# Optimization experiments

Measured on AMD Instinct MI355X. Metric: run time of the kernel, lower is better.

The kernel has to match this reference:

```python
import jax, jax.numpy as jnp
import numpy as np

B, S, D_IN = 4, 2048, 1024
D_OUT, H = 1024, 16
HD = D_OUT // H  # head_dim = 64

def setup_inputs() -> dict:
    key = jax.random.key(0)
    ks = jax.random.split(key, 6)
    scale_in = 1.0 / np.sqrt(D_IN)
    scale_out = 1.0 / np.sqrt(D_OUT)
    return {
        "x": jax.random.normal(ks[0], (B, S, D_IN), dtype=jnp.float32),
        "Wq": jax.random.uniform(ks[1], (D_OUT, D_IN), jnp.float32, -scale_in, scale_in),
        "Wk": jax.random.uniform(ks[2], (D_OUT, D_IN), jnp.float32, -scale_in, scale_in),
        "Wv": jax.random.uniform(ks[3], (D_OUT, D_IN), jnp.float32, -scale_in, scale_in),
        "Wo": jax.random.uniform(ks[4], (D_OUT, D_OUT), jnp.float32, -scale_out, scale_out),
        "bo": jax.random.uniform(ks[5], (D_OUT,), jnp.float32, -scale_out, scale_out),
    }

def reference(x, Wq, Wk, Wv, Wo, bo):
    b, s, _ = x.shape
    # projections (nn.Linear: x @ W.T), split into heads -> [b, h, s, hd]
    def proj(W):
        return jnp.einsum('bsd,ed->bse', x, W).reshape(b, s, H, HD).transpose(0, 2, 1, 3)
    q, k, v = proj(Wq), proj(Wk), proj(Wv)
    # full score matrix [b, h, s, s] with causal mask, scaled softmax
    scores = jnp.einsum('bhqd,bhkd->bhqk', q, k)
    causal = jnp.tril(jnp.ones((s, s), dtype=bool))
    scores = jnp.where(causal, scores, -jnp.inf)
    attn = jax.nn.softmax(scores / np.sqrt(HD), axis=-1)
    # dropout p=0.0 -> identity
    ctx = jnp.einsum('bhqk,bhkd->bqhd', attn, v).reshape(b, s, D_OUT)
    return jnp.einsum('bsd,ed->bse', ctx, Wo) + bo
```

## Files before the change

### kernel.cpp

```cpp
#include <hip/hip_runtime.h>
#include <cstdint>
#include <cstddef>

#define S_LEN   2048
#define D_MODEL 1024
#define N_HEADS 16
#define HEAD_DIM 64
#define BATCH   4
#define M_ROWS  (BATCH * S_LEN)

typedef _Float16 half8  __attribute__((ext_vector_type(8)));
typedef _Float16 half4v __attribute__((ext_vector_type(4)));
typedef float    float4v __attribute__((ext_vector_type(4)));

#define AS1 __attribute__((address_space(1)))
#define AS3 __attribute__((address_space(3)))

#define QSCL 0.1803368801111832f

__device__ __forceinline__ int swz(int row, int byteInRow) {
    return row * 128 + ((((byteInRow >> 4) ^ (row & 7)) << 4)) + (byteInRow & 15);
}

__device__ __forceinline__ int vperm(int a) {
    return (a & 0x20) | ((a & 0x0C) << 1) | ((a & 0x10) >> 2) | (a & 3);
}

__global__ __launch_bounds__(256) void cvt_all(const float* __restrict__ x,
                                               const float* __restrict__ wq,
                                               const float* __restrict__ wk,
                                               const float* __restrict__ wv,
                                               const float* __restrict__ wo,
                                               _Float16* __restrict__ dst) {
    const int NX = M_ROWS * D_MODEL / 4;
    const int NW = D_MODEL * D_MODEL / 4;
    int i = blockIdx.x * 256 + threadIdx.x;
    int j = i;
    const float4v* src;
    if (j < NX) src = (const float4v*)x;
    else {
        j -= NX;
        if (j < NW) src = (const float4v*)wq;
        else { j -= NW;
            if (j < NW) src = (const float4v*)wk;
            else { j -= NW;
                if (j < NW) src = (const float4v*)wv;
                else { j -= NW; src = (const float4v*)wo; }
            }
        }
    }
    float4v v = src[j];
    half4v h;
    h[0] = (_Float16)v[0]; h[1] = (_Float16)v[1];
    h[2] = (_Float16)v[2]; h[3] = (_Float16)v[3];
    ((half4v*)dst)[i] = h;
}

#define GK   1024
#define GNT  16
#define BUFB 49152
#define GEMM_LDS (3 * BUFB)

template <int MODE>
__global__ __launch_bounds__(512, 2) void gemm8p(const _Float16* __restrict__ A,
                                                 const _Float16* __restrict__ Bw,
                                                 _Float16* __restrict__ O1,
                                                 _Float16* __restrict__ O2,
                                                 float* __restrict__ Of,
                                                 const float* __restrict__ bias,
                                                 int N) {
    extern __shared__ char smem[];

    const int tid  = threadIdx.x;
    const int wave = tid >> 6;
    const int lane = tid & 63;
    const int quad = lane >> 4;
    const int l16  = lane & 15;
    const int wm   = wave >> 1;
    const int wn   = wave & 1;

    const int rowBase = blockIdx.x * 256;
    const int colBase = blockIdx.y * 128;

    const int srow = tid >> 3;
    const int csw  = ((tid & 7) ^ (srow & 7)) * 8;
    const _Float16* aS[4];
    const _Float16* bS[2];
#pragma unroll
    for (int i = 0; i < 4; ++i)
        aS[i] = A + (size_t)(rowBase + i * 64 + srow) * GK + csw;
#pragma unroll
    for (int j = 0; j < 2; ++j)
        bS[j] = Bw + (size_t)(colBase + j * 64 + srow) * GK + csw;
    const int dstOff = tid * 16;

    auto stage = [&](int kt, int part) {
        char* base = smem + (kt % 3) * BUFB;
        const size_t ko = (size_t)kt * 64;
        if (part == 0) {
            __builtin_amdgcn_global_load_lds((const AS1 void*)(aS[0] + ko),
                (AS3 void*)(base + 0 * 8192 + dstOff), 16, 0, 0);
            __builtin_amdgcn_global_load_lds((const AS1 void*)(aS[1] + ko),
                (AS3 void*)(base + 1 * 8192 + dstOff), 16, 0, 0);
            __builtin_amdgcn_global_load_lds((const AS1 void*)(bS[0] + ko),
                (AS3 void*)(base + 32768 + dstOff), 16, 0, 0);
        } else {
            __builtin_amdgcn_global_load_lds((const AS1 void*)(aS[2] + ko),
                (AS3 void*)(base + 2 * 8192 + dstOff), 16, 0, 0);
            __builtin_amdgcn_global_load_lds((const AS1 void*)(aS[3] + ko),
                (AS3 void*)(base + 3 * 8192 + dstOff), 16, 0, 0);
            __builtin_amdgcn_global_load_lds((const AS1 void*)(bS[1] + ko),
                (AS3 void*)(base + 32768 + 8192 + dstOff), 16, 0, 0);
        }
    };

    const int aRow = (wm * 64 + l16) * 128;
    const int bRow = (wn * 64 + l16) * 128;
    int swzk[2];
    swzk[0] = ((quad)     ^ (l16 & 7)) << 4;
    swzk[1] = ((quad + 4) ^ (l16 & 7)) << 4;

    float4v acc[4][4] = {};

    stage(0, 0); stage(0, 1); stage(1, 0); stage(1, 1);
    asm volatile("s_waitcnt vmcnt(6)" ::: "memory");
    __builtin_amdgcn_s_barrier();

#pragma unroll
    for (int kt = 0; kt < GNT; ++kt) {
        const char* Ab = smem + (kt % 3) * BUFB;
        const char* Bb = Ab + 32768;
#pragma unroll
        for (int ks = 0; ks < 2; ++ks) {
            half8 af[4], bf[4];
#pragma unroll
            for (int mi = 0; mi < 4; ++mi)
                af[mi] = *(const half8*)(Ab + aRow + mi * 2048 + swzk[ks]);
#pragma unroll
            for (int ni = 0; ni < 4; ++ni)
                bf[ni] = *(const half8*)(Bb + bRow + ni * 2048 + swzk[ks]);
            if (kt + 2 < GNT) stage(kt + 2, ks);
            __builtin_amdgcn_s_barrier();
            asm volatile("s_waitcnt lgkmcnt(0)" ::: "memory");
            __builtin_amdgcn_sched_barrier(0);
            __builtin_amdgcn_s_setprio(1);
#pragma unroll
            for (int mi = 0; mi < 4; ++mi)
#pragma unroll
                for (int ni = 0; ni < 4; ++ni)
                    acc[mi][ni] = __builtin_amdgcn_mfma_f32_16x16x32_f16(
                        af[mi], bf[ni], acc[mi][ni], 0, 0, 0);
            __builtin_amdgcn_s_setprio(0);
            if (ks == 1) {
                if (kt + 2 < GNT) {
                    asm volatile("s_waitcnt vmcnt(6)" ::: "memory");
                } else if (kt + 1 < GNT) {
                    asm volatile("s_waitcnt vmcnt(0)" ::: "memory");
                }
            }
            __builtin_amdgcn_s_barrier();
        }
    }

    const int rowOff = wm * 64;
    const int colOff = wn * 64;
#pragma unroll
    for (int mi = 0; mi < 4; ++mi)
#pragma unroll
        for (int ni = 0; ni < 4; ++ni) {
            const int col = colBase + colOff + ni * 16 + l16;
#pragma unroll
            for (int i = 0; i < 4; ++i) {
                const int row = rowBase + rowOff + mi * 16 + quad * 4 + i;
                float v = acc[mi][ni][i];
                if (MODE == 0) {
                    int b_ = row >> 11, s_ = row & 2047;
                    int proj = col >> 10, d = col & 1023;
                    int h_ = d >> 6, hd = d & 63;
                    _Float16* dst = proj ? O2 : O1;
                    if (proj == 0) v *= QSCL;
                    dst[(((size_t)(b_ * 16 + h_) * 2048 + s_) << 6) + hd] = (_Float16)v;
                } else if (MODE == 1) {
                    int h_ = row >> 6, hd = row & 63;
                    int b_ = col >> 11, s_ = col & 2047;
                    int sp = (s_ & ~63) | vperm(s_ & 63);
                    O1[(((size_t)(b_ * 16 + h_) * 64 + hd) << 11) + sp] = (_Float16)v;
                } else {
                    Of[(size_t)row * N + col] = v + bias[col];
                }
            }
        }
}

template <bool MASKED>
__device__ __forceinline__ void attn_step5(const half8 qf[2],
                                           const _Float16* __restrict__ Ks,
                                           const _Float16* __restrict__ Vs,
                                           int krow0, int qt, int quad, int c,
                                           float4v o[4], float& l) {
    float4v sT[4] = {};
    __builtin_amdgcn_s_setprio(1);
#pragma unroll
    for (int nt = 0; nt < 4; ++nt)
#pragma unroll
        for (int ks = 0; ks < 2; ++ks) {
            half8 kf = *(const half8*)((const char*)Ks + swz(nt * 16 + c, ks * 64 + quad * 16));
            sT[nt] = __builtin_amdgcn_mfma_f32_16x16x32_f16(kf, qf[ks], sT[nt], 0, 0, 0);
        }
    __builtin_amdgcn_s_setprio(0);

    const int qrow_g = qt + c;
#pragma unroll
    for (int kk = 0; kk < 2; ++kk) {
        float e[2][4];
#pragma unroll
        for (int jh = 0; jh < 2; ++jh) {
            const int nt = 2 * kk + jh;
#pragma unroll
            for (int i = 0; i < 4; ++i) {
                float ev = __builtin_amdgcn_exp2f(sT[nt][i]);
                if (MASKED)
                    ev = (krow0 + nt * 16 + quad * 4 + i <= qrow_g) ? ev : 0.0f;
                e[jh][i] = ev;
                l += ev;
            }
        }
        auto p0 = __builtin_amdgcn_cvt_pkrtz(e[0][0], e[0][1]);
        auto p1 = __builtin_amdgcn_cvt_pkrtz(e[0][2], e[0][3]);
        auto p2 = __builtin_amdgcn_cvt_pkrtz(e[1][0], e[1][1]);
        auto p3 = __builtin_amdgcn_cvt_pkrtz(e[1][2], e[1][3]);
        half8 pf;
        pf[0] = p0[0]; pf[1] = p0[1]; pf[2] = p1[0]; pf[3] = p1[1];
        pf[4] = p2[0]; pf[5] = p2[1]; pf[6] = p3[0]; pf[7] = p3[1];
        __builtin_amdgcn_s_setprio(1);
#pragma unroll
        for (int dt = 0; dt < 4; ++dt) {
            half8 vf = *(const half8*)((const char*)Vs + swz(dt * 16 + c, kk * 64 + quad * 16));
            o[dt] = __builtin_amdgcn_mfma_f32_16x16x32_f16(pf, vf, o[dt], 0, 0, 0);
        }
        __builtin_amdgcn_s_setprio(0);
    }
}

__global__ __launch_bounds__(256, 4) void attn_flash5(const _Float16* __restrict__ Q,
                                                      const _Float16* __restrict__ Kg,
                                                      const _Float16* __restrict__ Vt,
                                                      _Float16* __restrict__ Ctx) {
    __shared__ __align__(16) _Float16 Ks[2 * 64 * 64];
    __shared__ __align__(16) _Float16 Vs[2 * 64 * 64];

    const int tid  = threadIdx.x;
    const int wave = tid >> 6;
    const int lane = tid & 63;
    const int quad = lane >> 4;
    const int c    = lane & 15;

    const int h    = blockIdx.x;
    const int hp   = blockIdx.y;
    const int bb   = blockIdx.z;
    const int pair = hp >> 1;
    const int hf   = hp & 1;

    const int qA = pair * 128 + hf * 64 + wave * 16;
    const int qB = (15 - pair) * 128 + hf * 64 + wave * 16;
    const int nkbB = (15 - pair) * 2 + hf + 1;

    const _Float16* Qb  = Q  + ((size_t)(bb * 16 + h) << 17);
    const _Float16* Kb  = Kg + ((size_t)(bb * 16 + h) << 17);
    const _Float16* Vtb = Vt + ((size_t)(bb * 16 + h) << 17);

    half8 qfA[2], qfB[2];
    {
        const _Float16* qa = Qb + (size_t)(qA + c) * 64;
        qfA[0] = *(const half8*)(qa + quad * 8);
        qfA[1] = *(const half8*)(qa + 32 + quad * 8);
        const _Float16* qb = Qb + (size_t)(qB + c) * 64;
        qfB[0] = *(const half8*)(qb + quad * 8);
        qfB[1] = *(const half8*)(qb + 32 + quad * 8);
    }

    size_t koff[2], voff[2];
#pragma unroll
    for (int it = 0; it < 2; ++it) {
        int F = it * 4096 + tid * 16;
        int r = F >> 7;
        int blk = (tid & 7) ^ (r & 7);
        koff[it] = (size_t)r * 64 + blk * 8;
        voff[it] = (size_t)r * 2048 + blk * 8;
    }

    float4v oA[4] = {}, oB[4] = {};
    float lA = 0.0f, lB = 0.0f;

    auto stage = [&](int kb, int buf) {
        const size_t kbase = (size_t)kb * 64 * 64;
#pragma unroll
        for (int it = 0; it < 2; ++it) {
            __builtin_amdgcn_global_load_lds(
                (const AS1 void*)(Kb + kbase + koff[it]),
                (AS3 void*)((char*)Ks + buf * 8192 + it * 4096 + wave * 1024), 16, 0, 0);
            __builtin_amdgcn_global_load_lds(
                (const AS1 void*)(Vtb + kb * 64 + voff[it]),
                (AS3 void*)((char*)Vs + buf * 8192 + it * 4096 + wave * 1024), 16, 0, 0);
        }
    };

    stage(0, 0);
    for (int kb = 0; kb < nkbB; ++kb) {
        __syncthreads();
        if (kb + 1 < nkbB) stage(kb + 1, (kb + 1) & 1);

        const _Float16* Ksb = Ks + (kb & 1) * 4096;
        const _Float16* Vsb = Vs + (kb & 1) * 4096;
        const int krow0 = kb * 64;

        if (krow0 <= qB + 15) {
            if (krow0 + 63 <= qB)
                attn_step5<false>(qfB, Ksb, Vsb, krow0, qB, quad, c, oB, lB);
            else
                attn_step5<true >(qfB, Ksb, Vsb, krow0, qB, quad, c, oB, lB);
        }
        if (krow0 <= qA + 15) {
            if (krow0 + 63 <= qA)
                attn_step5<false>(qfA, Ksb, Vsb, krow0, qA, quad, c, oA, lA);
            else
                attn_step5<true >(qfA, Ksb, Vsb, krow0, qA, quad, c, oA, lA);
        }
    }

    lA += __shfl_xor(lA, 16); lA += __shfl_xor(lA, 32);
    lB += __shfl_xor(lB, 16); lB += __shfl_xor(lB, 32);

#pragma unroll
    for (int t = 0; t < 2; ++t) {
        const float lv = t ? lB : lA;
        float4v* o = t ? oB : oA;
        const int qt = t ? qB : qA;
#pragma unroll
        for (int i = 0; i < 4; ++i) {
            const float inv = 1.0f / __shfl(lv, quad * 4 + i);
            const int row_g = qt + quad * 4 + i;
            _Float16* dst = Ctx + (size_t)(bb * 2048 + row_g) * 1024 + h * 64;
#pragma unroll
            for (int dt = 0; dt < 4; ++dt)
                dst[dt * 16 + c] = (_Float16)(o[dt][i] * inv);
        }
    }
}

extern "C" void kernel_launch(void* const* d_in, const int* in_sizes, int n_in,
                              void* d_out, int out_size, void* d_ws, size_t ws_size,
                              hipStream_t stream) {
    const float* x  = (const float*)d_in[0];
    const float* Wq = (const float*)d_in[1];
    const float* Wk = (const float*)d_in[2];
    const float* Wv = (const float*)d_in[3];
    const float* Wo = (const float*)d_in[4];
    const float* bo = (const float*)d_in[5];
    float* out = (float*)d_out;

    _Float16* Xh   = (_Float16*)d_ws;
    _Float16* Wqkh = Xh + (size_t)M_ROWS * D_MODEL;
    _Float16* Wvh  = Wqkh + (size_t)2 * D_MODEL * D_MODEL;
    _Float16* Woh  = Wvh + (size_t)D_MODEL * D_MODEL;
    _Float16* Qh   = Woh + (size_t)D_MODEL * D_MODEL;
    _Float16* Kh   = Qh + (size_t)M_ROWS * D_MODEL;
    _Float16* Vth  = Kh + (size_t)M_ROWS * D_MODEL;
    _Float16* Ch   = Vth + (size_t)M_ROWS * D_MODEL;

    static bool s_init = false;
    if (!s_init) {
        hipFuncSetAttribute((const void*)gemm8p<0>,
                            hipFuncAttributeMaxDynamicSharedMemorySize, GEMM_LDS);
        hipFuncSetAttribute((const void*)gemm8p<1>,
                            hipFuncAttributeMaxDynamicSharedMemorySize, GEMM_LDS);
        hipFuncSetAttribute((const void*)gemm8p<2>,
                            hipFuncAttributeMaxDynamicSharedMemorySize, GEMM_LDS);
        s_init = true;
    }

    const int TOT4 = (M_ROWS * D_MODEL + 4 * D_MODEL * D_MODEL) / 4;
    cvt_all<<<TOT4 / 256, 256, 0, stream>>>(x, Wq, Wk, Wv, Wo, Xh);

    gemm8p<0><<<dim3(M_ROWS / 256, 2048 / 128), 512, GEMM_LDS, stream>>>(
        Xh, Wqkh, Qh, Kh, nullptr, nullptr, 2048);
    gemm8p<1><<<dim3(D_MODEL / 256, M_ROWS / 128), 512, GEMM_LDS, stream>>>(
        Wvh, Xh, Vth, nullptr, nullptr, nullptr, M_ROWS);

    attn_flash5<<<dim3(N_HEADS, 16, BATCH), 256, 0, stream>>>(Qh, Kh, Vth, Ch);

    gemm8p<2><<<dim3(M_ROWS / 256, D_MODEL / 128), 512, GEMM_LDS, stream>>>(
        Ch, Woh, nullptr, nullptr, out, bo, D_MODEL);
}
```

Baseline: 153.8 us.

## Restructure attention so each wave handles 32 query rows with shared K/V fragments

The attention kernel moves from 4 waves of 16 query rows each to 2 waves of 32 rows each (128 threads per block). K fragments are loaded from LDS once per tile and reused across both 16-row subtiles and both paired query blocks. V fragments are likewise loaded once and applied to all four accumulators. Row sums are now computed with an MFMA against a vector of ones instead of scalar adds and cross-lane shuffles. Per-wave register pressure goes up and the kernel runs fewer waves per block, which may lower occupancy and latency hiding.

```diff
diff --git a/kernel.cpp b/kernel.cpp
--- a/kernel.cpp
+++ b/kernel.cpp
@@ -193,56 +193,41 @@
 }
 
 template <bool MASKED>
-__device__ __forceinline__ void attn_step5(const half8 qf[2],
-                                           const _Float16* __restrict__ Ks,
-                                           const _Float16* __restrict__ Vs,
-                                           int krow0, int qt, int quad, int c,
-                                           float4v o[4], float& l) {
-    float4v sT[4] = {};
-    __builtin_amdgcn_s_setprio(1);
-#pragma unroll
-    for (int nt = 0; nt < 4; ++nt)
-#pragma unroll
-        for (int ks = 0; ks < 2; ++ks) {
-            half8 kf = *(const half8*)((const char*)Ks + swz(nt * 16 + c, ks * 64 + quad * 16));
-            sT[nt] = __builtin_amdgcn_mfma_f32_16x16x32_f16(kf, qf[ks], sT[nt], 0, 0, 0);
-        }
-    __builtin_amdgcn_s_setprio(0);
-
-    const int qrow_g = qt + c;
-#pragma unroll
-    for (int kk = 0; kk < 2; ++kk) {
-        float e[2][4];
-#pragma unroll
-        for (int jh = 0; jh < 2; ++jh) {
-            const int nt = 2 * kk + jh;
-#pragma unroll
-            for (int i = 0; i < 4; ++i) {
-                float ev = __builtin_amdgcn_exp2f(sT[nt][i]);
-                if (MASKED)
-                    ev = (krow0 + nt * 16 + quad * 4 + i <= qrow_g) ? ev : 0.0f;
-                e[jh][i] = ev;
-                l += ev;
-            }
-        }
-        auto p0 = __builtin_amdgcn_cvt_pkrtz(e[0][0], e[0][1]);
-        auto p1 = __builtin_amdgcn_cvt_pkrtz(e[0][2], e[0][3]);
-        auto p2 = __builtin_amdgcn_cvt_pkrtz(e[1][0], e[1][1]);
-        auto p3 = __builtin_amdgcn_cvt_pkrtz(e[1][2], e[1][3]);
-        half8 pf;
-        pf[0] = p0[0]; pf[1] = p0[1]; pf[2] = p1[0]; pf[3] = p1[1];
-        pf[4] = p2[0]; pf[5] = p2[1]; pf[6] = p3[0]; pf[7] = p3[1];
-        __builtin_amdgcn_s_setprio(1);
-#pragma unroll
-        for (int dt = 0; dt < 4; ++dt) {
-            half8 vf = *(const half8*)((const char*)Vs + swz(dt * 16 + c, kk * 64 + quad * 16));
-            o[dt] = __builtin_amdgcn_mfma_f32_16x16x32_f16(pf, vf, o[dt], 0, 0, 0);
-        }
-        __builtin_amdgcn_s_setprio(0);
-    }
-}
-
-__global__ __launch_bounds__(256, 4) void attn_flash5(const _Float16* __restrict__ Q,
+__device__ __forceinline__ void softmax_side(const float4v (&sT)[2][4], int krow0,
+                                             int qt, int quad, int c,
+                                             half8 (&pf)[2][2], float4v (&ol)[2],
+                                             half8 ones) {
+#pragma unroll
+    for (int s = 0; s < 2; ++s) {
+        const int qrow = qt + s * 16 + c;
+#pragma unroll
+        for (int kk = 0; kk < 2; ++kk) {
+            float e[2][4];
+#pragma unroll
+            for (int jh = 0; jh < 2; ++jh) {
+                const int nt = 2 * kk + jh;
+#pragma unroll
+                for (int i = 0; i < 4; ++i) {
+                    float ev = __builtin_amdgcn_exp2f(sT[s][nt][i]);
+                    if (MASKED)
+                        ev = (krow0 + nt * 16 + quad * 4 + i <= qrow) ? ev : 0.0f;
+                    e[jh][i] = ev;
+                }
+            }
+            auto p0 = __builtin_amdgcn_cvt_pkrtz(e[0][0], e[0][1]);
+            auto p1 = __builtin_amdgcn_cvt_pkrtz(e[0][2], e[0][3]);
+            auto p2 = __builtin_amdgcn_cvt_pkrtz(e[1][0], e[1][1]);
+            auto p3 = __builtin_amdgcn_cvt_pkrtz(e[1][2], e[1][3]);
+            half8 pfv;
+            pfv[0] = p0[0]; pfv[1] = p0[1]; pfv[2] = p1[0]; pfv[3] = p1[1];
+            pfv[4] = p2[0]; pfv[5] = p2[1]; pfv[6] = p3[0]; pfv[7] = p3[1];
+            pf[s][kk] = pfv;
+            ol[s] = __builtin_amdgcn_mfma_f32_16x16x32_f16(pfv, ones, ol[s], 0, 0, 0);
+        }
+    }
+}
+
+__global__ __launch_bounds__(128, 2) void attn_flash7(const _Float16* __restrict__ Q,
                                                       const _Float16* __restrict__ Kg,
                                                       const _Float16* __restrict__ Vt,
                                                       _Float16* __restrict__ Ctx) {
@@ -255,95 +240,162 @@
     const int quad = lane >> 4;
     const int c    = lane & 15;
 
-    const int h    = blockIdx.x;
+    const int h    = blockIdx.x & 15;
+    const int bb   = blockIdx.x >> 4;
     const int hp   = blockIdx.y;
-    const int bb   = blockIdx.z;
     const int pair = hp >> 1;
     const int hf   = hp & 1;
 
-    const int qA = pair * 128 + hf * 64 + wave * 16;
-    const int qB = (15 - pair) * 128 + hf * 64 + wave * 16;
-    const int nkbB = (15 - pair) * 2 + hf + 1;
+    const int qA  = pair * 128 + hf * 64 + wave * 32;
+    const int qB  = (15 - pair) * 128 + hf * 64 + wave * 32;
+    const int nkb = 2 * (15 - pair) + hf + 1;
 
     const _Float16* Qb  = Q  + ((size_t)(bb * 16 + h) << 17);
     const _Float16* Kb  = Kg + ((size_t)(bb * 16 + h) << 17);
     const _Float16* Vtb = Vt + ((size_t)(bb * 16 + h) << 17);
 
-    half8 qfA[2], qfB[2];
-    {
-        const _Float16* qa = Qb + (size_t)(qA + c) * 64;
-        qfA[0] = *(const half8*)(qa + quad * 8);
-        qfA[1] = *(const half8*)(qa + 32 + quad * 8);
-        const _Float16* qb = Qb + (size_t)(qB + c) * 64;
-        qfB[0] = *(const half8*)(qb + quad * 8);
-        qfB[1] = *(const half8*)(qb + 32 + quad * 8);
-    }
-
-    size_t koff[2], voff[2];
-#pragma unroll
-    for (int it = 0; it < 2; ++it) {
-        int F = it * 4096 + tid * 16;
+    half8 qfA[2][2], qfB[2][2];
+#pragma unroll
+    for (int s = 0; s < 2; ++s) {
+        const _Float16* qa = Qb + (size_t)(qA + s * 16 + c) * 64;
+        qfA[s][0] = *(const half8*)(qa + quad * 8);
+        qfA[s][1] = *(const half8*)(qa + 32 + quad * 8);
+        const _Float16* qb = Qb + (size_t)(qB + s * 16 + c) * 64;
+        qfB[s][0] = *(const half8*)(qb + quad * 8);
+        qfB[s][1] = *(const half8*)(qb + 32 + quad * 8);
+    }
+
+    size_t koff[4], voff[4];
+#pragma unroll
+    for (int it = 0; it < 4; ++it) {
+        int F = it * 2048 + tid * 16;
         int r = F >> 7;
-        int blk = (tid & 7) ^ (r & 7);
+        int blk = ((F >> 4) & 7) ^ (r & 7);
         koff[it] = (size_t)r * 64 + blk * 8;
         voff[it] = (size_t)r * 2048 + blk * 8;
     }
 
-    float4v oA[4] = {}, oB[4] = {};
-    float lA = 0.0f, lB = 0.0f;
+    float4v oB[2][4] = {}, oA[2][4] = {};
+    float4v olB[2] = {}, olA[2] = {};
+    half8 ones;
+#pragma unroll
+    for (int i = 0; i < 8; ++i) ones[i] = (_Float16)1.0f;
 
     auto stage = [&](int kb, int buf) {
         const size_t kbase = (size_t)kb * 64 * 64;
 #pragma unroll
-        for (int it = 0; it < 2; ++it) {
+        for (int it = 0; it < 4; ++it) {
             __builtin_amdgcn_global_load_lds(
                 (const AS1 void*)(Kb + kbase + koff[it]),
-                (AS3 void*)((char*)Ks + buf * 8192 + it * 4096 + wave * 1024), 16, 0, 0);
+                (AS3 void*)((char*)Ks + buf * 8192 + it * 2048 + wave * 1024), 16, 0, 0);
             __builtin_amdgcn_global_load_lds(
                 (const AS1 void*)(Vtb + kb * 64 + voff[it]),
-                (AS3 void*)((char*)Vs + buf * 8192 + it * 4096 + wave * 1024), 16, 0, 0);
+                (AS3 void*)((char*)Vs + buf * 8192 + it * 2048 + wave * 1024), 16, 0, 0);
         }
     };
 
+    const int g0 = ((quad ^ (c & 7)) << 4);
+    const int g1 = (((quad ^ 4) ^ (c & 7)) << 4);
+
     stage(0, 0);
-    for (int kb = 0; kb < nkbB; ++kb) {
+    for (int kb = 0; kb < nkb; ++kb) {
         __syncthreads();
-        if (kb + 1 < nkbB) stage(kb + 1, (kb + 1) & 1);
-
-        const _Float16* Ksb = Ks + (kb & 1) * 4096;
-        const _Float16* Vsb = Vs + (kb & 1) * 4096;
+        if (kb + 1 < nkb) stage(kb + 1, (kb + 1) & 1);
+
+        const char* base  = (const char*)Ks + (kb & 1) * 8192;
+        const char* vbase = (const char*)Vs + (kb & 1) * 8192;
+        const char* b0 = base + c * 128 + g0;
+        const char* b1 = base + c * 128 + g1;
         const int krow0 = kb * 64;
-
-        if (krow0 <= qB + 15) {
+        const bool aB = krow0 <= qB + 31;
+        const bool aA = krow0 <= qA + 31;
+
+        half8 kfr[4][2];
+#pragma unroll
+        for (int nt = 0; nt < 4; ++nt) {
+            kfr[nt][0] = *(const half8*)(b0 + nt * 2048);
+            kfr[nt][1] = *(const half8*)(b1 + nt * 2048);
+        }
+
+        half8 pfB[2][2], pfA[2][2];
+        if (aB) {
+            float4v sT[2][4] = {};
+            __builtin_amdgcn_s_setprio(1);
+#pragma unroll
+            for (int nt = 0; nt < 4; ++nt)
+#pragma unroll
+                for (int s = 0; s < 2; ++s) {
+                    sT[s][nt] = __builtin_amdgcn_mfma_f32_16x16x32_f16(
+                        kfr[nt][0], qfB[s][0], sT[s][nt], 0, 0, 0);
+                    sT[s][nt] = __builtin_amdgcn_mfma_f32_16x16x32_f16(
+                        kfr[nt][1], qfB[s][1], sT[s][nt], 0, 0, 0);
+                }
+            __builtin_amdgcn_s_setprio(0);
             if (krow0 + 63 <= qB)
-                attn_step5<false>(qfB, Ksb, Vsb, krow0, qB, quad, c, oB, lB);
+                softmax_side<false>(sT, krow0, qB, quad, c, pfB, olB, ones);
             else
-                attn_step5<true >(qfB, Ksb, Vsb, krow0, qB, quad, c, oB, lB);
-        }
-        if (krow0 <= qA + 15) {
+                softmax_side<true >(sT, krow0, qB, quad, c, pfB, olB, ones);
+        }
+        if (aA) {
+            float4v sT[2][4] = {};
+            __builtin_amdgcn_s_setprio(1);
+#pragma unroll
+            for (int nt = 0; nt < 4; ++nt)
+#pragma unroll
+                for (int s = 0; s < 2; ++s) {
+                    sT[s][nt] = __builtin_amdgcn_mfma_f32_16x16x32_f16(
+                        kfr[nt][0], qfA[s][0], sT[s][nt], 0, 0, 0);
+                    sT[s][nt] = __builtin_amdgcn_mfma_f32_16x16x32_f16(
+                        kfr[nt][1], qfA[s][1], sT[s][nt], 0, 0, 0);
+                }
+            __builtin_amdgcn_s_setprio(0);
             if (krow0 + 63 <= qA)
-                attn_step5<false>(qfA, Ksb, Vsb, krow0, qA, quad, c, oA, lA);
+                softmax_side<false>(sT, krow0, qA, quad, c, pfA, olA, ones);
             else
-                attn_step5<true >(qfA, Ksb, Vsb, krow0, qA, quad, c, oA, lA);
-        }
-    }
-
-    lA += __shfl_xor(lA, 16); lA += __shfl_xor(lA, 32);
-    lB += __shfl_xor(lB, 16); lB += __shfl_xor(lB, 32);
+                softmax_side<true >(sT, krow0, qA, quad, c, pfA, olA, ones);
+        }
+
+        const char* v0 = vbase + c * 128 + g0;
+        const char* v1 = vbase + c * 128 + g1;
+#pragma unroll
+        for (int kk = 0; kk < 2; ++kk) {
+            const char* vb = kk ? v1 : v0;
+#pragma unroll
+            for (int dt = 0; dt < 4; ++dt) {
+                half8 vf = *(const half8*)(vb + dt * 2048);
+                if (aB) {
+                    oB[0][dt] = __builtin_amdgcn_mfma_f32_16x16x32_f16(
+                        pfB[0][kk], vf, oB[0][dt], 0, 0, 0);
+                    oB[1][dt] = __builtin_amdgcn_mfma_f32_16x16x32_f16(
+                        pfB[1][kk], vf, oB[1][dt], 0, 0, 0);
+                }
+                if (aA) {
+                    oA[0][dt] = __builtin_amdgcn_mfma_f32_16x16x32_f16(
+                        pfA[0][kk], vf, oA[0][dt], 0, 0, 0);
+                    oA[1][dt] = __builtin_amdgcn_mfma_f32_16x16x32_f16(
+                        pfA[1][kk], vf, oA[1][dt], 0, 0, 0);
+                }
+            }
+        }
+    }
 
 #pragma unroll
     for (int t = 0; t < 2; ++t) {
-        const float lv = t ? lB : lA;
-        float4v* o = t ? oB : oA;
         const int qt = t ? qB : qA;
 #pragma unroll
-        for (int i = 0; i < 4; ++i) {
-            const float inv = 1.0f / __shfl(lv, quad * 4 + i);
-            const int row_g = qt + quad * 4 + i;
-            _Float16* dst = Ctx + (size_t)(bb * 2048 + row_g) * 1024 + h * 64;
-#pragma unroll
-            for (int dt = 0; dt < 4; ++dt)
-                dst[dt * 16 + c] = (_Float16)(o[dt][i] * inv);
+        for (int s = 0; s < 2; ++s) {
+#pragma unroll
+            for (int i = 0; i < 4; ++i) {
+                const float lsum = t ? olB[s][i] : olA[s][i];
+                const float inv = 1.0f / lsum;
+                const int row_g = qt + s * 16 + quad * 4 + i;
+                _Float16* dst = Ctx + (size_t)(bb * 2048 + row_g) * 1024 + h * 64;
+#pragma unroll
+                for (int dt = 0; dt < 4; ++dt) {
+                    const float ov = t ? oB[s][dt][i] : oA[s][dt][i];
+                    dst[dt * 16 + c] = (_Float16)(ov * inv);
+                }
+            }
         }
     }
 }
@@ -387,7 +439,7 @@
     gemm8p<1><<<dim3(D_MODEL / 256, M_ROWS / 128), 512, GEMM_LDS, stream>>>(
         Wvh, Xh, Vth, nullptr, nullptr, nullptr, M_ROWS);
 
-    attn_flash5<<<dim3(N_HEADS, 16, BATCH), 256, 0, stream>>>(Qh, Kh, Vth, Ch);
+    attn_flash7<<<dim3(64, 16), 128, 0, stream>>>(Qh, Kh, Vth, Ch);
 
     gemm8p<2><<<dim3(M_ROWS / 256, D_MODEL / 128), 512, GEMM_LDS, stream>>>(
         Ch, Woh, nullptr, nullptr, out, bo, D_MODEL);
```

Result: slower. 157.1 us (+2.1%).

## Compute softmax row sums via MFMA and share V fragment loads across query tiles

Applied to the files above, without the earlier changes.

The attention kernel now computes the row sums of exp scores with an MFMA against a vector of ones, replacing scalar accumulation and the cross-lane shuffle reduction. The PV stage is hoisted out of the per-tile helper so each V fragment read from LDS feeds both query tiles A and B, halving V LDS reads. Block-to-work mapping is also permuted so heavy and light causal tiles interleave across launch order. The ones-MFMA adds matrix work and the fp16-rounded probabilities now feed the sum, which changes normalization slightly. Both tiles' probability fragments are kept live at once, which raises register pressure.

```diff
diff --git a/kernel.cpp b/kernel.cpp
--- a/kernel.cpp
+++ b/kernel.cpp
@@ -193,11 +193,10 @@
 }
 
 template <bool MASKED>
-__device__ __forceinline__ void attn_step5(const half8 qf[2],
-                                           const _Float16* __restrict__ Ks,
-                                           const _Float16* __restrict__ Vs,
-                                           int krow0, int qt, int quad, int c,
-                                           float4v o[4], float& l) {
+__device__ __forceinline__ void qk_sm(const half8 qf[2],
+                                      const _Float16* __restrict__ Ks,
+                                      int krow0, int qt, int quad, int c,
+                                      half8 (&pf)[2], float4v& ol, half8 ones) {
     float4v sT[4] = {};
     __builtin_amdgcn_s_setprio(1);
 #pragma unroll
@@ -209,7 +208,7 @@
         }
     __builtin_amdgcn_s_setprio(0);
 
-    const int qrow_g = qt + c;
+    const int qrow = qt + c;
 #pragma unroll
     for (int kk = 0; kk < 2; ++kk) {
         float e[2][4];
@@ -220,32 +219,26 @@
             for (int i = 0; i < 4; ++i) {
                 float ev = __builtin_amdgcn_exp2f(sT[nt][i]);
                 if (MASKED)
-                    ev = (krow0 + nt * 16 + quad * 4 + i <= qrow_g) ? ev : 0.0f;
+                    ev = (krow0 + nt * 16 + quad * 4 + i <= qrow) ? ev : 0.0f;
                 e[jh][i] = ev;
-                l += ev;
             }
         }
         auto p0 = __builtin_amdgcn_cvt_pkrtz(e[0][0], e[0][1]);
         auto p1 = __builtin_amdgcn_cvt_pkrtz(e[0][2], e[0][3]);
         auto p2 = __builtin_amdgcn_cvt_pkrtz(e[1][0], e[1][1]);
         auto p3 = __builtin_amdgcn_cvt_pkrtz(e[1][2], e[1][3]);
-        half8 pf;
-        pf[0] = p0[0]; pf[1] = p0[1]; pf[2] = p1[0]; pf[3] = p1[1];
-        pf[4] = p2[0]; pf[5] = p2[1]; pf[6] = p3[0]; pf[7] = p3[1];
-        __builtin_amdgcn_s_setprio(1);
-#pragma unroll
-        for (int dt = 0; dt < 4; ++dt) {
-            half8 vf = *(const half8*)((const char*)Vs + swz(dt * 16 + c, kk * 64 + quad * 16));
-            o[dt] = __builtin_amdgcn_mfma_f32_16x16x32_f16(pf, vf, o[dt], 0, 0, 0);
-        }
-        __builtin_amdgcn_s_setprio(0);
-    }
-}
-
-__global__ __launch_bounds__(256, 4) void attn_flash5(const _Float16* __restrict__ Q,
-                                                      const _Float16* __restrict__ Kg,
-                                                      const _Float16* __restrict__ Vt,
-                                                      _Float16* __restrict__ Ctx) {
+        half8 pfv;
+        pfv[0] = p0[0]; pfv[1] = p0[1]; pfv[2] = p1[0]; pfv[3] = p1[1];
+        pfv[4] = p2[0]; pfv[5] = p2[1]; pfv[6] = p3[0]; pfv[7] = p3[1];
+        pf[kk] = pfv;
+        ol = __builtin_amdgcn_mfma_f32_16x16x32_f16(pfv, ones, ol, 0, 0, 0);
+    }
+}
+
+__global__ __launch_bounds__(256, 4) void attn_flash10(const _Float16* __restrict__ Q,
+                                                       const _Float16* __restrict__ Kg,
+                                                       const _Float16* __restrict__ Vt,
+                                                       _Float16* __restrict__ Ctx) {
     __shared__ __align__(16) _Float16 Ks[2 * 64 * 64];
     __shared__ __align__(16) _Float16 Vs[2 * 64 * 64];
 
@@ -256,13 +249,14 @@
     const int c    = lane & 15;
 
     const int h    = blockIdx.x;
-    const int hp   = blockIdx.y;
+    const int y    = blockIdx.y;
     const int bb   = blockIdx.z;
+    const int hp   = (y < 8) ? y : 23 - y;
     const int pair = hp >> 1;
     const int hf   = hp & 1;
 
-    const int qA = pair * 128 + hf * 64 + wave * 16;
-    const int qB = (15 - pair) * 128 + hf * 64 + wave * 16;
+    const int qA   = pair * 128 + hf * 64 + wave * 16;
+    const int qB   = (15 - pair) * 128 + hf * 64 + wave * 16;
     const int nkbB = (15 - pair) * 2 + hf + 1;
 
     const _Float16* Qb  = Q  + ((size_t)(bb * 16 + h) << 17);
@@ -290,7 +284,10 @@
     }
 
     float4v oA[4] = {}, oB[4] = {};
-    float lA = 0.0f, lB = 0.0f;
+    float4v olA = {}, olB = {};
+    half8 ones;
+#pragma unroll
+    for (int i = 0; i < 8; ++i) ones[i] = (_Float16)1.0f;
 
     auto stage = [&](int kb, int buf) {
         const size_t kbase = (size_t)kb * 64 * 64;
@@ -313,37 +310,53 @@
         const _Float16* Ksb = Ks + (kb & 1) * 4096;
         const _Float16* Vsb = Vs + (kb & 1) * 4096;
         const int krow0 = kb * 64;
-
-        if (krow0 <= qB + 15) {
+        const bool aB = krow0 <= qB + 15;
+        const bool aA = krow0 <= qA + 15;
+
+        half8 pfB[2], pfA[2];
+        if (aB) {
             if (krow0 + 63 <= qB)
-                attn_step5<false>(qfB, Ksb, Vsb, krow0, qB, quad, c, oB, lB);
+                qk_sm<false>(qfB, Ksb, krow0, qB, quad, c, pfB, olB, ones);
             else
-                attn_step5<true >(qfB, Ksb, Vsb, krow0, qB, quad, c, oB, lB);
-        }
-        if (krow0 <= qA + 15) {
+                qk_sm<true >(qfB, Ksb, krow0, qB, quad, c, pfB, olB, ones);
+        }
+        if (aA) {
             if (krow0 + 63 <= qA)
-                attn_step5<false>(qfA, Ksb, Vsb, krow0, qA, quad, c, oA, lA);
+                qk_sm<false>(qfA, Ksb, krow0, qA, quad, c, pfA, olA, ones);
             else
-                attn_step5<true >(qfA, Ksb, Vsb, krow0, qA, quad, c, oA, lA);
-        }
-    }
-
-    lA += __shfl_xor(lA, 16); lA += __shfl_xor(lA, 32);
-    lB += __shfl_xor(lB, 16); lB += __shfl_xor(lB, 32);
+                qk_sm<true >(qfA, Ksb, krow0, qA, quad, c, pfA, olA, ones);
+        }
+
+        __builtin_amdgcn_s_setprio(1);
+#pragma unroll
+        for (int kk = 0; kk < 2; ++kk)
+#pragma unroll
+            for (int dt = 0; dt < 4; ++dt) {
+                half8 vf = *(const half8*)((const char*)Vsb + swz(dt * 16 + c, kk * 64 + quad * 16));
+                if (aB)
+                    oB[dt] = __builtin_amdgcn_mfma_f32_16x16x32_f16(
+                        pfB[kk], vf, oB[dt], 0, 0, 0);
+                if (aA)
+                    oA[dt] = __builtin_amdgcn_mfma_f32_16x16x32_f16(
+                        pfA[kk], vf, oA[dt], 0, 0, 0);
+            }
+        __builtin_amdgcn_s_setprio(0);
+    }
 
 #pragma unroll
     for (int t = 0; t < 2; ++t) {
-        const float lv = t ? lB : lA;
-        float4v* o = t ? oB : oA;
         const int qt = t ? qB : qA;
 #pragma unroll
         for (int i = 0; i < 4; ++i) {
-            const float inv = 1.0f / __shfl(lv, quad * 4 + i);
+            const float lsum = t ? olB[i] : olA[i];
+            const float inv = 1.0f / lsum;
             const int row_g = qt + quad * 4 + i;
             _Float16* dst = Ctx + (size_t)(bb * 2048 + row_g) * 1024 + h * 64;
 #pragma unroll
-            for (int dt = 0; dt < 4; ++dt)
-                dst[dt * 16 + c] = (_Float16)(o[dt][i] * inv);
+            for (int dt = 0; dt < 4; ++dt) {
+                const float ov = t ? oB[dt][i] : oA[dt][i];
+                dst[dt * 16 + c] = (_Float16)(ov * inv);
+            }
         }
     }
 }
@@ -387,7 +400,7 @@
     gemm8p<1><<<dim3(D_MODEL / 256, M_ROWS / 128), 512, GEMM_LDS, stream>>>(
         Wvh, Xh, Vth, nullptr, nullptr, nullptr, M_ROWS);
 
-    attn_flash5<<<dim3(N_HEADS, 16, BATCH), 256, 0, stream>>>(Qh, Kh, Vth, Ch);
+    attn_flash10<<<dim3(N_HEADS, 16, BATCH), 256, 0, stream>>>(Qh, Kh, Vth, Ch);
 
     gemm8p<2><<<dim3(M_ROWS / 256, D_MODEL / 128), 512, GEMM_LDS, stream>>>(
         Ch, Woh, nullptr, nullptr, out, bo, D_MODEL);
```

Result: slower. 157.8 us (+2.6%).

## Replace paired causal q-strips with one strip per block, heaviest first

Applied to the files above, without the earlier changes.

The attention kernel no longer gives each block two mirrored 64-row query strips for load balance. Each block now handles a single 64-row strip, and strips are launched from the last one down so the longest blocks are scheduled first. This doubles the grid to 2048 blocks and removes the per-iteration branching over two query sets. In exchange, K/V tiles are no longer shared between two strips in one block, so K/V traffic per unit of compute rises, and balance now depends on the hardware block scheduler.

```diff
diff --git a/kernel.cpp b/kernel.cpp
--- a/kernel.cpp
+++ b/kernel.cpp
@@ -242,10 +242,10 @@
     }
 }
 
-__global__ __launch_bounds__(256, 4) void attn_flash5(const _Float16* __restrict__ Q,
-                                                      const _Float16* __restrict__ Kg,
-                                                      const _Float16* __restrict__ Vt,
-                                                      _Float16* __restrict__ Ctx) {
+__global__ __launch_bounds__(256, 4) void attn_flash11(const _Float16* __restrict__ Q,
+                                                       const _Float16* __restrict__ Kg,
+                                                       const _Float16* __restrict__ Vt,
+                                                       _Float16* __restrict__ Ctx) {
     __shared__ __align__(16) _Float16 Ks[2 * 64 * 64];
     __shared__ __align__(16) _Float16 Vs[2 * 64 * 64];
 
@@ -255,28 +255,22 @@
     const int quad = lane >> 4;
     const int c    = lane & 15;
 
-    const int h    = blockIdx.x;
-    const int hp   = blockIdx.y;
-    const int bb   = blockIdx.z;
-    const int pair = hp >> 1;
-    const int hf   = hp & 1;
-
-    const int qA = pair * 128 + hf * 64 + wave * 16;
-    const int qB = (15 - pair) * 128 + hf * 64 + wave * 16;
-    const int nkbB = (15 - pair) * 2 + hf + 1;
+    const int h     = blockIdx.x;
+    const int strip = 31 - blockIdx.y;
+    const int bb    = blockIdx.z;
+
+    const int qt  = strip * 64 + wave * 16;
+    const int nkb = strip + 1;
 
     const _Float16* Qb  = Q  + ((size_t)(bb * 16 + h) << 17);
     const _Float16* Kb  = Kg + ((size_t)(bb * 16 + h) << 17);
     const _Float16* Vtb = Vt + ((size_t)(bb * 16 + h) << 17);
 
-    half8 qfA[2], qfB[2];
+    half8 qf[2];
     {
-        const _Float16* qa = Qb + (size_t)(qA + c) * 64;
-        qfA[0] = *(const half8*)(qa + quad * 8);
-        qfA[1] = *(const half8*)(qa + 32 + quad * 8);
-        const _Float16* qb = Qb + (size_t)(qB + c) * 64;
-        qfB[0] = *(const half8*)(qb + quad * 8);
-        qfB[1] = *(const half8*)(qb + 32 + quad * 8);
+        const _Float16* qa = Qb + (size_t)(qt + c) * 64;
+        qf[0] = *(const half8*)(qa + quad * 8);
+        qf[1] = *(const half8*)(qa + 32 + quad * 8);
     }
 
     size_t koff[2], voff[2];
@@ -289,8 +283,8 @@
         voff[it] = (size_t)r * 2048 + blk * 8;
     }
 
-    float4v oA[4] = {}, oB[4] = {};
-    float lA = 0.0f, lB = 0.0f;
+    float4v o[4] = {};
+    float l = 0.0f;
 
     auto stage = [&](int kb, int buf) {
         const size_t kbase = (size_t)kb * 64 * 64;
@@ -306,45 +300,30 @@
     };
 
     stage(0, 0);
-    for (int kb = 0; kb < nkbB; ++kb) {
+    for (int kb = 0; kb < nkb; ++kb) {
         __syncthreads();
-        if (kb + 1 < nkbB) stage(kb + 1, (kb + 1) & 1);
+        if (kb + 1 < nkb) stage(kb + 1, (kb + 1) & 1);
 
         const _Float16* Ksb = Ks + (kb & 1) * 4096;
         const _Float16* Vsb = Vs + (kb & 1) * 4096;
         const int krow0 = kb * 64;
 
-        if (krow0 <= qB + 15) {
-            if (krow0 + 63 <= qB)
-                attn_step5<false>(qfB, Ksb, Vsb, krow0, qB, quad, c, oB, lB);
-            else
-                attn_step5<true >(qfB, Ksb, Vsb, krow0, qB, quad, c, oB, lB);
-        }
-        if (krow0 <= qA + 15) {
-            if (krow0 + 63 <= qA)
-                attn_step5<false>(qfA, Ksb, Vsb, krow0, qA, quad, c, oA, lA);
-            else
-                attn_step5<true >(qfA, Ksb, Vsb, krow0, qA, quad, c, oA, lA);
-        }
-    }
-
-    lA += __shfl_xor(lA, 16); lA += __shfl_xor(lA, 32);
-    lB += __shfl_xor(lB, 16); lB += __shfl_xor(lB, 32);
-
-#pragma unroll
-    for (int t = 0; t < 2; ++t) {
-        const float lv = t ? lB : lA;
-        float4v* o = t ? oB : oA;
-        const int qt = t ? qB : qA;
-#pragma unroll
-        for (int i = 0; i < 4; ++i) {
-            const float inv = 1.0f / __shfl(lv, quad * 4 + i);
-            const int row_g = qt + quad * 4 + i;
-            _Float16* dst = Ctx + (size_t)(bb * 2048 + row_g) * 1024 + h * 64;
-#pragma unroll
-            for (int dt = 0; dt < 4; ++dt)
-                dst[dt * 16 + c] = (_Float16)(o[dt][i] * inv);
-        }
+        if (kb == strip)
+            attn_step5<true >(qf, Ksb, Vsb, krow0, qt, quad, c, o, l);
+        else
+            attn_step5<false>(qf, Ksb, Vsb, krow0, qt, quad, c, o, l);
+    }
+
+    l += __shfl_xor(l, 16); l += __shfl_xor(l, 32);
+
+#pragma unroll
+    for (int i = 0; i < 4; ++i) {
+        const float inv = 1.0f / __shfl(l, quad * 4 + i);
+        const int row_g = qt + quad * 4 + i;
+        _Float16* dst = Ctx + (size_t)(bb * 2048 + row_g) * 1024 + h * 64;
+#pragma unroll
+        for (int dt = 0; dt < 4; ++dt)
+            dst[dt * 16 + c] = (_Float16)(o[dt][i] * inv);
     }
 }
 
@@ -387,7 +366,7 @@
     gemm8p<1><<<dim3(D_MODEL / 256, M_ROWS / 128), 512, GEMM_LDS, stream>>>(
         Wvh, Xh, Vth, nullptr, nullptr, nullptr, M_ROWS);
 
-    attn_flash5<<<dim3(N_HEADS, 16, BATCH), 256, 0, stream>>>(Qh, Kh, Vth, Ch);
+    attn_flash11<<<dim3(N_HEADS, 32, BATCH), 256, 0, stream>>>(Qh, Kh, Vth, Ch);
 
     gemm8p<2><<<dim3(M_ROWS / 256, D_MODEL / 128), 512, GEMM_LDS, stream>>>(
         Ch, Woh, nullptr, nullptr, out, bo, D_MODEL);
```

New measurement: 160.1 us. +4.1%, slower.
